# Kernel tuning notes

Hardware: AMD Instinct MI355X
Metric: run time of the kernel (lower is better)

The kernel has to match this reference:

```python
import jax, jax.numpy as jnp
import numpy as np

N = 262144   # total sentences
B = 16384    # number of bags
D = 768      # relation_dim
C = 53       # num_classes


def setup_inputs() -> dict:
    key = jax.random.key(0)
    k1, k2, k3, k4 = jax.random.split(key, 4)
    x = jax.random.normal(k1, (N, D), dtype=jnp.float32)
    # xavier_uniform-like init for the relation embedding matrix [C, D]
    limit = float(np.sqrt(6.0 / (C + D)))
    rel_weight = jax.random.uniform(k2, (C, D), dtype=jnp.float32, minval=-limit, maxval=limit)
    bias = jax.random.normal(k3, (C,), dtype=jnp.float32)
    query = jax.random.randint(k4, (N,), 0, C, dtype=jnp.int32)
    # uniform bag boundaries: 0, 16, 32, ..., N  (len B+1)
    input_scope = (jnp.arange(B + 1, dtype=jnp.int32) * (N // B)).astype(jnp.int32)
    return {"x": x, "rel_weight": rel_weight, "bias": bias,
            "input_scope": input_scope, "query": query}


def reference(x, rel_weight, bias, input_scope, query):
    n = x.shape[0]
    num_bags = input_scope.shape[0] - 1
    # segment id of each sentence from bag boundaries (ragged -> segment form)
    seg = jnp.searchsorted(input_scope[1:], jnp.arange(n, dtype=input_scope.dtype), side="right")
    # _train_logits: per-sentence attention score <x_i, rel_emb[query_i]>
    att = jnp.sum(x * rel_weight[query], axis=1)                  # [N]
    # segment-stable softmax within each bag
    m = jax.ops.segment_max(att, seg, num_segments=num_bags)      # [B]
    e = jnp.exp(att - m[seg])                                     # [N]
    z = jax.ops.segment_sum(e, seg, num_segments=num_bags)        # [B]
    w = e / z[seg]                                                # [N]
    # attention-weighted bag representation
    repre = jax.ops.segment_sum(x * w[:, None], seg, num_segments=num_bags)  # [B, D]
    # _logits: bag representation -> class logits
    logits = repre @ rel_weight.T + bias                          # [B, C]
    return logits
```

## Files before the change

### kernel.cpp

```cpp
#include <hip/hip_runtime.h>
#include <hip/hip_bf16.h>

#define DIM    768
#define NC     53
#define NCP    64
#define MTB    256
#define NTH    512
#define NSTEPS 24

typedef __attribute__((ext_vector_type(8))) short short8;
typedef __attribute__((ext_vector_type(4))) float f32x4;

static __device__ inline unsigned short f2bf(float f) {
    unsigned u = __float_as_uint(f);
    u += 0x7fff + ((u >> 16) & 1);
    return (unsigned short)(u >> 16);
}

__global__ void wconv_kernel(const float* __restrict__ W, unsigned short* __restrict__ Wt) {
    const int idx = blockIdx.x * 256 + threadIdx.x;
    if (idx >= NCP * DIM) return;
    const int c = idx / DIM, k = idx - c * DIM;
    Wt[idx] = f2bf((c < NC) ? W[c * DIM + k] : 0.f);
}

static __device__ inline short8 cvt8(const float4 a, const float4 b) {
    union { __hip_bfloat162 h[4]; short8 s; } u;
    u.h[0] = __float22bfloat162_rn(make_float2(a.x, a.y));
    u.h[1] = __float22bfloat162_rn(make_float2(a.z, a.w));
    u.h[2] = __float22bfloat162_rn(make_float2(b.x, b.y));
    u.h[3] = __float22bfloat162_rn(make_float2(b.z, b.w));
    return u.s;
}

__global__ __launch_bounds__(NTH, 4) void bag_attn_mfma2(
    const float* __restrict__ x,
    const unsigned short* __restrict__ Wt,
    const float* __restrict__ bias,
    const int*   __restrict__ query,
    float*       __restrict__ out)
{
    __shared__ float att_sm[16][16];

    const int t   = threadIdx.x;
    const int w   = t >> 6;
    const int l   = t & 63;
    const int blk = blockIdx.x;
    const int row_g = blk * MTB;

    const int r16 = l & 15;
    const int kq  = l >> 4;

    const float4* a0p = reinterpret_cast<const float4*>(x)
                      + (size_t)(row_g + 32 * w + r16) * (DIM / 4) + kq * 2;
    const float4* a1p = a0p + 16 * (DIM / 4);
    const unsigned short* wb = Wt + r16 * DIM + kq * 8;

    f32x4 acc[2][4];
    #pragma unroll
    for (int mi = 0; mi < 2; ++mi)
        #pragma unroll
        for (int ni = 0; ni < 4; ++ni)
            acc[mi][ni] = (f32x4){0.f, 0.f, 0.f, 0.f};

    float4 P0a = a0p[0], P0b = a0p[1], P1a = a1p[0], P1b = a1p[1];
    float4 Q0a = a0p[8], Q0b = a0p[9], Q1a = a1p[8], Q1b = a1p[9];

    #pragma unroll
    for (int kk = 0; kk < NSTEPS; kk += 2) {
        {
            const short8 af0 = cvt8(P0a, P0b);
            const short8 af1 = cvt8(P1a, P1b);
            if (kk + 2 < NSTEPS) {
                P0a = a0p[(kk + 2) * 8 + 0]; P0b = a0p[(kk + 2) * 8 + 1];
                P1a = a1p[(kk + 2) * 8 + 0]; P1b = a1p[(kk + 2) * 8 + 1];
            }
            #pragma unroll
            for (int ni = 0; ni < 4; ++ni) {
                const short8 bf = *reinterpret_cast<const short8*>(
                    wb + ni * 16 * DIM + kk * 32);
                acc[0][ni] = __builtin_amdgcn_mfma_f32_16x16x32_bf16(af0, bf, acc[0][ni], 0, 0, 0);
                acc[1][ni] = __builtin_amdgcn_mfma_f32_16x16x32_bf16(af1, bf, acc[1][ni], 0, 0, 0);
            }
        }
        {
            const short8 ag0 = cvt8(Q0a, Q0b);
            const short8 ag1 = cvt8(Q1a, Q1b);
            if (kk + 3 < NSTEPS) {
                Q0a = a0p[(kk + 3) * 8 + 0]; Q0b = a0p[(kk + 3) * 8 + 1];
                Q1a = a1p[(kk + 3) * 8 + 0]; Q1b = a1p[(kk + 3) * 8 + 1];
            }
            #pragma unroll
            for (int ni = 0; ni < 4; ++ni) {
                const short8 bf = *reinterpret_cast<const short8*>(
                    wb + ni * 16 * DIM + (kk + 1) * 32);
                acc[0][ni] = __builtin_amdgcn_mfma_f32_16x16x32_bf16(ag0, bf, acc[0][ni], 0, 0, 0);
                acc[1][ni] = __builtin_amdgcn_mfma_f32_16x16x32_bf16(ag1, bf, acc[1][ni], 0, 0, 0);
            }
        }
    }

    #pragma unroll
    for (int mi = 0; mi < 2; ++mi) {
        #pragma unroll
        for (int r = 0; r < 4; ++r) {
            const int s_loc = (kq << 2) + r;
            const int q = query[row_g + 32 * w + 16 * mi + s_loc];
            if ((q & 15) == r16) {
                float v = acc[mi][0][r];
                if ((q >> 4) == 1) v = acc[mi][1][r];
                if ((q >> 4) == 2) v = acc[mi][2][r];
                if ((q >> 4) == 3) v = acc[mi][3][r];
                att_sm[2 * w + mi][s_loc] = v;
            }
        }
    }

    #pragma unroll
    for (int mi = 0; mi < 2; ++mi) {
        const int bag = 2 * w + mi;
        const float4* a4 = reinterpret_cast<const float4*>(&att_sm[bag][0]);
        const float4 A0 = a4[0], A1 = a4[1], A2 = a4[2], A3 = a4[3];
        float mx = fmaxf(fmaxf(fmaxf(A0.x, A0.y), fmaxf(A0.z, A0.w)),
                  fmaxf(fmaxf(fmaxf(A1.x, A1.y), fmaxf(A1.z, A1.w)),
                  fmaxf(fmaxf(fmaxf(A2.x, A2.y), fmaxf(A2.z, A2.w)),
                        fmaxf(fmaxf(A3.x, A3.y), fmaxf(A3.z, A3.w)))));
        float zz = __expf(A0.x-mx)+__expf(A0.y-mx)+__expf(A0.z-mx)+__expf(A0.w-mx)
                 + __expf(A1.x-mx)+__expf(A1.y-mx)+__expf(A1.z-mx)+__expf(A1.w-mx)
                 + __expf(A2.x-mx)+__expf(A2.y-mx)+__expf(A2.z-mx)+__expf(A2.w-mx)
                 + __expf(A3.x-mx)+__expf(A3.y-mx)+__expf(A3.z-mx)+__expf(A3.w-mx);
        const float inv = 1.f / zz;
        float4 As = A0;
        if (kq == 1) As = A1;
        if (kq == 2) As = A2;
        if (kq == 3) As = A3;
        const float w0 = __expf(As.x - mx) * inv;
        const float w1 = __expf(As.y - mx) * inv;
        const float w2 = __expf(As.z - mx) * inv;
        const float w3 = __expf(As.w - mx) * inv;
        #pragma unroll
        for (int ni = 0; ni < 4; ++ni) {
            float p = w0 * acc[mi][ni][0] + w1 * acc[mi][ni][1]
                    + w2 * acc[mi][ni][2] + w3 * acc[mi][ni][3];
            p += __shfl_xor(p, 16, 64);
            p += __shfl_xor(p, 32, 64);
            if (l < 16) {
                const int c = 16 * ni + l;
                if (c < NC)
                    out[(size_t)(blk * 16 + bag) * NC + c] = p + bias[c];
            }
        }
    }
}

extern "C" void kernel_launch(void* const* d_in, const int* in_sizes, int n_in,
                              void* d_out, int out_size, void* d_ws, size_t ws_size,
                              hipStream_t stream) {
    const float* x     = (const float*)d_in[0];
    const float* W     = (const float*)d_in[1];
    const float* bias  = (const float*)d_in[2];
    const int*   query = (const int*)d_in[4];
    float* out = (float*)d_out;

    unsigned short* Wt = (unsigned short*)d_ws;

    const int nrows = in_sizes[0] / DIM;
    const int nblk  = nrows / MTB;

    wconv_kernel<<<(NCP * DIM + 255) / 256, 256, 0, stream>>>(W, Wt);
    bag_attn_mfma2<<<nblk, NTH, 0, stream>>>(x, Wt, bias, query, out);
}
```

Measured before the change: 212.6 us.

## Split block into producer and consumer waves with double-buffered LDS staging

The block is split into two roles. Four producer waves load x from global memory, convert it to bf16 and write it into a double-buffered, padded LDS tile, one bag per phase. Four consumer waves each compute one 16-class slice of the logits with MFMA, then run the bag softmax and write the weighted output. The aim is to overlap global loads with MFMA work, but it adds a block-wide barrier every phase and leaves half the waves doing no compute.

```diff
diff --git a/kernel.cpp b/kernel.cpp
--- a/kernel.cpp
+++ b/kernel.cpp
@@ -1,12 +1,14 @@
 #include <hip/hip_runtime.h>
 #include <hip/hip_bf16.h>
 
-#define DIM    768
-#define NC     53
-#define NCP    64
-#define MTB    256
-#define NTH    512
-#define NSTEPS 24
+#define DIM   768
+#define NC    53
+#define NCP   64
+#define MTB   256
+#define NTH   512
+#define NPH   16
+#define LSTR  776
+#define LBUF  (16 * LSTR)
 
 typedef __attribute__((ext_vector_type(8))) short short8;
 typedef __attribute__((ext_vector_type(4))) float f32x4;
@@ -24,130 +26,127 @@
     Wt[idx] = f2bf((c < NC) ? W[c * DIM + k] : 0.f);
 }
 
-static __device__ inline short8 cvt8(const float4 a, const float4 b) {
-    union { __hip_bfloat162 h[4]; short8 s; } u;
-    u.h[0] = __float22bfloat162_rn(make_float2(a.x, a.y));
-    u.h[1] = __float22bfloat162_rn(make_float2(a.z, a.w));
-    u.h[2] = __float22bfloat162_rn(make_float2(b.x, b.y));
-    u.h[3] = __float22bfloat162_rn(make_float2(b.z, b.w));
-    return u.s;
+static __device__ inline void cvt_store8(unsigned short* dst, const float4 v) {
+    union { __hip_bfloat162 h[2]; uint2 u; } z;
+    z.h[0] = __float22bfloat162_rn(make_float2(v.x, v.y));
+    z.h[1] = __float22bfloat162_rn(make_float2(v.z, v.w));
+    *reinterpret_cast<uint2*>(dst) = z.u;
 }
 
-__global__ __launch_bounds__(NTH, 4) void bag_attn_mfma2(
+__global__ __launch_bounds__(NTH) void bag_attn_pc(
     const float* __restrict__ x,
     const unsigned short* __restrict__ Wt,
     const float* __restrict__ bias,
     const int*   __restrict__ query,
     float*       __restrict__ out)
 {
-    __shared__ float att_sm[16][16];
+    __shared__ __align__(16) unsigned short Ab[2][LBUF];
+    __shared__ float att_sm[2][16];
+    __shared__ int   qbuf[MTB];
 
     const int t   = threadIdx.x;
     const int w   = t >> 6;
     const int l   = t & 63;
+    const int r16 = l & 15;
+    const int kq  = l >> 4;
     const int blk = blockIdx.x;
     const int row_g = blk * MTB;
 
-    const int r16 = l & 15;
-    const int kq  = l >> 4;
+    if (t < MTB) qbuf[t] = query[row_g + t];
 
-    const float4* a0p = reinterpret_cast<const float4*>(x)
-                      + (size_t)(row_g + 32 * w + r16) * (DIM / 4) + kq * 2;
-    const float4* a1p = a0p + 16 * (DIM / 4);
-    const unsigned short* wb = Wt + r16 * DIM + kq * 8;
+    const bool prod = (w >= 4);
+    const int  pid  = w - 4;
 
-    f32x4 acc[2][4];
-    #pragma unroll
-    for (int mi = 0; mi < 2; ++mi)
+    const float* xb = x + (size_t)row_g * DIM;
+    float4 rg[12];
+    int    lofs[12];
+    if (prod) {
         #pragma unroll
-        for (int ni = 0; ni < 4; ++ni)
-            acc[mi][ni] = (f32x4){0.f, 0.f, 0.f, 0.f};
+        for (int j = 0; j < 12; ++j) {
+            const int c = pid * 12 + j;
+            lofs[j] = (c / 3) * LSTR + (c % 3) * 256 + l * 4;
+        }
+        #pragma unroll
+        for (int j = 0; j < 12; ++j) {
+            const int c = pid * 12 + j;
+            rg[j] = *reinterpret_cast<const float4*>(
+                xb + (size_t)(c / 3) * DIM + (c % 3) * 256 + l * 4);
+        }
+        #pragma unroll
+        for (int j = 0; j < 12; ++j)
+            cvt_store8(&Ab[0][lofs[j]], rg[j]);
+        #pragma unroll
+        for (int j = 0; j < 12; ++j) {
+            const int c = pid * 12 + j;
+            rg[j] = *reinterpret_cast<const float4*>(
+                xb + (size_t)(16 + c / 3) * DIM + (c % 3) * 256 + l * 4);
+        }
+    }
+    const unsigned short* wb = Wt + (size_t)(16 * w + r16) * DIM + kq * 8;
 
-    float4 P0a = a0p[0], P0b = a0p[1], P1a = a1p[0], P1b = a1p[1];
-    float4 Q0a = a0p[8], Q0b = a0p[9], Q1a = a1p[8], Q1b = a1p[9];
+    __syncthreads();
 
-    #pragma unroll
-    for (int kk = 0; kk < NSTEPS; kk += 2) {
-        {
-            const short8 af0 = cvt8(P0a, P0b);
-            const short8 af1 = cvt8(P1a, P1b);
-            if (kk + 2 < NSTEPS) {
-                P0a = a0p[(kk + 2) * 8 + 0]; P0b = a0p[(kk + 2) * 8 + 1];
-                P1a = a1p[(kk + 2) * 8 + 0]; P1b = a1p[(kk + 2) * 8 + 1];
+    for (int p = 0; p < NPH; ++p) {
+        f32x4 acc = (f32x4){0.f, 0.f, 0.f, 0.f};
+        if (prod) {
+            if (p + 1 < NPH) {
+                #pragma unroll
+                for (int j = 0; j < 12; ++j)
+                    cvt_store8(&Ab[(p + 1) & 1][lofs[j]], rg[j]);
+            }
+            if (p + 2 < NPH) {
+                #pragma unroll
+                for (int j = 0; j < 12; ++j) {
+                    const int c = pid * 12 + j;
+                    rg[j] = *reinterpret_cast<const float4*>(
+                        xb + (size_t)((p + 2) * 16 + c / 3) * DIM
+                           + (c % 3) * 256 + l * 4);
+                }
+            }
+        } else {
+            const unsigned short* ab = &Ab[p & 1][r16 * LSTR + kq * 8];
+            #pragma unroll
+            for (int kk = 0; kk < 24; ++kk) {
+                const short8 a = *reinterpret_cast<const short8*>(ab + kk * 32);
+                const short8 b = *reinterpret_cast<const short8*>(wb + kk * 32);
+                acc = __builtin_amdgcn_mfma_f32_16x16x32_bf16(a, b, acc, 0, 0, 0);
             }
             #pragma unroll
-            for (int ni = 0; ni < 4; ++ni) {
-                const short8 bf = *reinterpret_cast<const short8*>(
-                    wb + ni * 16 * DIM + kk * 32);
-                acc[0][ni] = __builtin_amdgcn_mfma_f32_16x16x32_bf16(af0, bf, acc[0][ni], 0, 0, 0);
-                acc[1][ni] = __builtin_amdgcn_mfma_f32_16x16x32_bf16(af1, bf, acc[1][ni], 0, 0, 0);
+            for (int r = 0; r < 4; ++r) {
+                const int s = kq * 4 + r;
+                const int q = qbuf[p * 16 + s];
+                if ((q >> 4) == w && (q & 15) == r16)
+                    att_sm[p & 1][s] = acc[r];
             }
         }
-        {
-            const short8 ag0 = cvt8(Q0a, Q0b);
-            const short8 ag1 = cvt8(Q1a, Q1b);
-            if (kk + 3 < NSTEPS) {
-                Q0a = a0p[(kk + 3) * 8 + 0]; Q0b = a0p[(kk + 3) * 8 + 1];
-                Q1a = a1p[(kk + 3) * 8 + 0]; Q1b = a1p[(kk + 3) * 8 + 1];
-            }
-            #pragma unroll
-            for (int ni = 0; ni < 4; ++ni) {
-                const short8 bf = *reinterpret_cast<const short8*>(
-                    wb + ni * 16 * DIM + (kk + 1) * 32);
-                acc[0][ni] = __builtin_amdgcn_mfma_f32_16x16x32_bf16(ag0, bf, acc[0][ni], 0, 0, 0);
-                acc[1][ni] = __builtin_amdgcn_mfma_f32_16x16x32_bf16(ag1, bf, acc[1][ni], 0, 0, 0);
-            }
-        }
-    }
-
-    #pragma unroll
-    for (int mi = 0; mi < 2; ++mi) {
-        #pragma unroll
-        for (int r = 0; r < 4; ++r) {
-            const int s_loc = (kq << 2) + r;
-            const int q = query[row_g + 32 * w + 16 * mi + s_loc];
-            if ((q & 15) == r16) {
-                float v = acc[mi][0][r];
-                if ((q >> 4) == 1) v = acc[mi][1][r];
-                if ((q >> 4) == 2) v = acc[mi][2][r];
-                if ((q >> 4) == 3) v = acc[mi][3][r];
-                att_sm[2 * w + mi][s_loc] = v;
-            }
-        }
-    }
-
-    #pragma unroll
-    for (int mi = 0; mi < 2; ++mi) {
-        const int bag = 2 * w + mi;
-        const float4* a4 = reinterpret_cast<const float4*>(&att_sm[bag][0]);
-        const float4 A0 = a4[0], A1 = a4[1], A2 = a4[2], A3 = a4[3];
-        float mx = fmaxf(fmaxf(fmaxf(A0.x, A0.y), fmaxf(A0.z, A0.w)),
-                  fmaxf(fmaxf(fmaxf(A1.x, A1.y), fmaxf(A1.z, A1.w)),
-                  fmaxf(fmaxf(fmaxf(A2.x, A2.y), fmaxf(A2.z, A2.w)),
-                        fmaxf(fmaxf(A3.x, A3.y), fmaxf(A3.z, A3.w)))));
-        float zz = __expf(A0.x-mx)+__expf(A0.y-mx)+__expf(A0.z-mx)+__expf(A0.w-mx)
-                 + __expf(A1.x-mx)+__expf(A1.y-mx)+__expf(A1.z-mx)+__expf(A1.w-mx)
-                 + __expf(A2.x-mx)+__expf(A2.y-mx)+__expf(A2.z-mx)+__expf(A2.w-mx)
-                 + __expf(A3.x-mx)+__expf(A3.y-mx)+__expf(A3.z-mx)+__expf(A3.w-mx);
-        const float inv = 1.f / zz;
-        float4 As = A0;
-        if (kq == 1) As = A1;
-        if (kq == 2) As = A2;
-        if (kq == 3) As = A3;
-        const float w0 = __expf(As.x - mx) * inv;
-        const float w1 = __expf(As.y - mx) * inv;
-        const float w2 = __expf(As.z - mx) * inv;
-        const float w3 = __expf(As.w - mx) * inv;
-        #pragma unroll
-        for (int ni = 0; ni < 4; ++ni) {
-            float p = w0 * acc[mi][ni][0] + w1 * acc[mi][ni][1]
-                    + w2 * acc[mi][ni][2] + w3 * acc[mi][ni][3];
-            p += __shfl_xor(p, 16, 64);
-            p += __shfl_xor(p, 32, 64);
+        __syncthreads();
+        if (!prod) {
+            const float4* a4 = reinterpret_cast<const float4*>(&att_sm[p & 1][0]);
+            const float4 A0 = a4[0], A1 = a4[1], A2 = a4[2], A3 = a4[3];
+            float mx = fmaxf(fmaxf(fmaxf(A0.x, A0.y), fmaxf(A0.z, A0.w)),
+                      fmaxf(fmaxf(fmaxf(A1.x, A1.y), fmaxf(A1.z, A1.w)),
+                      fmaxf(fmaxf(fmaxf(A2.x, A2.y), fmaxf(A2.z, A2.w)),
+                            fmaxf(fmaxf(A3.x, A3.y), fmaxf(A3.z, A3.w)))));
+            float zz = __expf(A0.x-mx)+__expf(A0.y-mx)+__expf(A0.z-mx)+__expf(A0.w-mx)
+                     + __expf(A1.x-mx)+__expf(A1.y-mx)+__expf(A1.z-mx)+__expf(A1.w-mx)
+                     + __expf(A2.x-mx)+__expf(A2.y-mx)+__expf(A2.z-mx)+__expf(A2.w-mx)
+                     + __expf(A3.x-mx)+__expf(A3.y-mx)+__expf(A3.z-mx)+__expf(A3.w-mx);
+            const float inv = 1.f / zz;
+            float4 As = A0;
+            if (kq == 1) As = A1;
+            if (kq == 2) As = A2;
+            if (kq == 3) As = A3;
+            const float e0 = __expf(As.x - mx) * inv;
+            const float e1 = __expf(As.y - mx) * inv;
+            const float e2 = __expf(As.z - mx) * inv;
+            const float e3 = __expf(As.w - mx) * inv;
+            float pv = e0 * acc[0] + e1 * acc[1] + e2 * acc[2] + e3 * acc[3];
+            pv += __shfl_xor(pv, 16, 64);
+            pv += __shfl_xor(pv, 32, 64);
             if (l < 16) {
-                const int c = 16 * ni + l;
+                const int c = 16 * w + l;
                 if (c < NC)
-                    out[(size_t)(blk * 16 + bag) * NC + c] = p + bias[c];
+                    out[(size_t)(blk * 16 + p) * NC + c] = pv + bias[c];
             }
         }
     }
@@ -168,5 +167,5 @@
     const int nblk  = nrows / MTB;
 
     wconv_kernel<<<(NCP * DIM + 255) / 256, 256, 0, stream>>>(W, Wt);
-    bag_attn_mfma2<<<nblk, NTH, 0, stream>>>(x, Wt, bias, query, out);
+    bag_attn_pc<<<nblk, NTH, 0, stream>>>(x, Wt, bias, query, out);
 }
```

Result: slower. 318.8 us (+50.0%).

## Stage x tiles through per-wave double-buffered LDS with coalesced row loads

Applied to the files above, without the earlier changes.

Each wave now loads its 32 rows of x with 8 lanes covering 128 contiguous bytes per row. It converts them to bf16 and writes them into a padded, double-buffered LDS tile, then reads MFMA A fragments back from LDS. The old scheme had each lane fetch scattered 32-byte pieces straight into fragments. Because each wave reads only the rows it wrote, no block barriers are needed. Weight fragment loads are also software-pipelined, one step ahead. The cost is extra LDS traffic and about 40KB of LDS per block, which may limit occupancy.

```diff
diff --git a/kernel.cpp b/kernel.cpp
--- a/kernel.cpp
+++ b/kernel.cpp
@@ -6,7 +6,10 @@
 #define NCP    64
 #define MTB    256
 #define NTH    512
+#define KSTEP  32
 #define NSTEPS 24
+#define APAD   40
+#define D4     (DIM/4)
 
 typedef __attribute__((ext_vector_type(8))) short short8;
 typedef __attribute__((ext_vector_type(4))) float f32x4;
@@ -24,37 +27,34 @@
     Wt[idx] = f2bf((c < NC) ? W[c * DIM + k] : 0.f);
 }
 
-static __device__ inline short8 cvt8(const float4 a, const float4 b) {
-    union { __hip_bfloat162 h[4]; short8 s; } u;
-    u.h[0] = __float22bfloat162_rn(make_float2(a.x, a.y));
-    u.h[1] = __float22bfloat162_rn(make_float2(a.z, a.w));
-    u.h[2] = __float22bfloat162_rn(make_float2(b.x, b.y));
-    u.h[3] = __float22bfloat162_rn(make_float2(b.z, b.w));
-    return u.s;
+static __device__ inline void cvt_store8(unsigned short* dst, const float4 v) {
+    union { __hip_bfloat162 h[2]; uint2 u; } z;
+    z.h[0] = __float22bfloat162_rn(make_float2(v.x, v.y));
+    z.h[1] = __float22bfloat162_rn(make_float2(v.z, v.w));
+    *reinterpret_cast<uint2*>(dst) = z.u;
 }
 
-__global__ __launch_bounds__(NTH, 4) void bag_attn_mfma2(
+__global__ __launch_bounds__(NTH, 4) void bag_attn_nobar(
     const float* __restrict__ x,
     const unsigned short* __restrict__ Wt,
     const float* __restrict__ bias,
     const int*   __restrict__ query,
     float*       __restrict__ out)
 {
+    __shared__ __align__(16) unsigned short Ab[2][MTB * APAD];
     __shared__ float att_sm[16][16];
 
     const int t   = threadIdx.x;
     const int w   = t >> 6;
     const int l   = t & 63;
+    const int r16 = l & 15;
+    const int kq  = l >> 4;
     const int blk = blockIdx.x;
     const int row_g = blk * MTB;
 
-    const int r16 = l & 15;
-    const int kq  = l >> 4;
-
-    const float4* a0p = reinterpret_cast<const float4*>(x)
-                      + (size_t)(row_g + 32 * w + r16) * (DIM / 4) + kq * 2;
-    const float4* a1p = a0p + 16 * (DIM / 4);
-    const unsigned short* wb = Wt + r16 * DIM + kq * 8;
+    const float4* xp = reinterpret_cast<const float4*>(x)
+                     + (size_t)(row_g + 32 * w + (l >> 3)) * D4 + (l & 7);
+    const int lofs = (32 * w + (l >> 3)) * APAD + (l & 7) * 4;
 
     f32x4 acc[2][4];
     #pragma unroll
@@ -63,42 +63,61 @@
         for (int ni = 0; ni < 4; ++ni)
             acc[mi][ni] = (f32x4){0.f, 0.f, 0.f, 0.f};
 
-    float4 P0a = a0p[0], P0b = a0p[1], P1a = a1p[0], P1b = a1p[1];
-    float4 Q0a = a0p[8], Q0b = a0p[9], Q1a = a1p[8], Q1b = a1p[9];
+    const unsigned short* wbase = Wt + (size_t)r16 * DIM + kq * 8;
 
-    #pragma unroll
+#define LOADB(B, kk)                                                     \
+    _Pragma("unroll")                                                    \
+    for (int ni = 0; ni < 4; ++ni)                                       \
+        B[ni] = *reinterpret_cast<const short8*>(                        \
+            wbase + (size_t)(16 * ni) * DIM + (kk) * KSTEP);
+
+#define LOADX(R, kk)                                                     \
+    _Pragma("unroll")                                                    \
+    for (int i = 0; i < 4; ++i)                                          \
+        R[i] = xp[(size_t)i * 8 * D4 + (kk) * 8];
+
+#define STOREX(R, buf)                                                   \
+    _Pragma("unroll")                                                    \
+    for (int i = 0; i < 4; ++i)                                          \
+        cvt_store8(&Ab[buf][lofs + i * 8 * APAD], R[i]);
+
+#define COMPUTE(p, B)                                                    \
+    {                                                                    \
+        short8 afr[2];                                                   \
+        _Pragma("unroll")                                                \
+        for (int mi = 0; mi < 2; ++mi)                                   \
+            afr[mi] = *reinterpret_cast<const short8*>(                  \
+                &Ab[p][(32 * w + 16 * mi + r16) * APAD + kq * 8]);       \
+        _Pragma("unroll")                                                \
+        for (int mi = 0; mi < 2; ++mi)                                   \
+            _Pragma("unroll")                                            \
+            for (int ni = 0; ni < 4; ++ni)                               \
+                acc[mi][ni] = __builtin_amdgcn_mfma_f32_16x16x32_bf16(   \
+                    afr[mi], B[ni], acc[mi][ni], 0, 0, 0);               \
+    }
+
+    short8 bP[4], bQ[4];
+    float4 rA[4], rB[4];
+
+    LOADB(bP, 0);
+    LOADX(rA, 0);
+    LOADX(rB, 1);
+    STOREX(rA, 0);
+
     for (int kk = 0; kk < NSTEPS; kk += 2) {
-        {
-            const short8 af0 = cvt8(P0a, P0b);
-            const short8 af1 = cvt8(P1a, P1b);
-            if (kk + 2 < NSTEPS) {
-                P0a = a0p[(kk + 2) * 8 + 0]; P0b = a0p[(kk + 2) * 8 + 1];
-                P1a = a1p[(kk + 2) * 8 + 0]; P1b = a1p[(kk + 2) * 8 + 1];
-            }
-            #pragma unroll
-            for (int ni = 0; ni < 4; ++ni) {
-                const short8 bf = *reinterpret_cast<const short8*>(
-                    wb + ni * 16 * DIM + kk * 32);
-                acc[0][ni] = __builtin_amdgcn_mfma_f32_16x16x32_bf16(af0, bf, acc[0][ni], 0, 0, 0);
-                acc[1][ni] = __builtin_amdgcn_mfma_f32_16x16x32_bf16(af1, bf, acc[1][ni], 0, 0, 0);
-            }
-        }
-        {
-            const short8 ag0 = cvt8(Q0a, Q0b);
-            const short8 ag1 = cvt8(Q1a, Q1b);
-            if (kk + 3 < NSTEPS) {
-                Q0a = a0p[(kk + 3) * 8 + 0]; Q0b = a0p[(kk + 3) * 8 + 1];
-                Q1a = a1p[(kk + 3) * 8 + 0]; Q1b = a1p[(kk + 3) * 8 + 1];
-            }
-            #pragma unroll
-            for (int ni = 0; ni < 4; ++ni) {
-                const short8 bf = *reinterpret_cast<const short8*>(
-                    wb + ni * 16 * DIM + (kk + 1) * 32);
-                acc[0][ni] = __builtin_amdgcn_mfma_f32_16x16x32_bf16(ag0, bf, acc[0][ni], 0, 0, 0);
-                acc[1][ni] = __builtin_amdgcn_mfma_f32_16x16x32_bf16(ag1, bf, acc[1][ni], 0, 0, 0);
-            }
-        }
+        LOADB(bQ, kk + 1);
+        if (kk + 2 < NSTEPS) LOADX(rA, kk + 2);
+        COMPUTE(0, bP);
+        STOREX(rB, 1);
+        if (kk + 2 < NSTEPS) LOADB(bP, kk + 2);
+        if (kk + 3 < NSTEPS) LOADX(rB, kk + 3);
+        COMPUTE(1, bQ);
+        if (kk + 2 < NSTEPS) STOREX(rA, 0);
     }
+#undef LOADB
+#undef LOADX
+#undef STOREX
+#undef COMPUTE
 
     #pragma unroll
     for (int mi = 0; mi < 2; ++mi) {
@@ -134,14 +153,14 @@
         if (kq == 1) As = A1;
         if (kq == 2) As = A2;
         if (kq == 3) As = A3;
-        const float w0 = __expf(As.x - mx) * inv;
-        const float w1 = __expf(As.y - mx) * inv;
-        const float w2 = __expf(As.z - mx) * inv;
-        const float w3 = __expf(As.w - mx) * inv;
+        const float e0 = __expf(As.x - mx) * inv;
+        const float e1 = __expf(As.y - mx) * inv;
+        const float e2 = __expf(As.z - mx) * inv;
+        const float e3 = __expf(As.w - mx) * inv;
         #pragma unroll
         for (int ni = 0; ni < 4; ++ni) {
-            float p = w0 * acc[mi][ni][0] + w1 * acc[mi][ni][1]
-                    + w2 * acc[mi][ni][2] + w3 * acc[mi][ni][3];
+            float p = e0 * acc[mi][ni][0] + e1 * acc[mi][ni][1]
+                    + e2 * acc[mi][ni][2] + e3 * acc[mi][ni][3];
             p += __shfl_xor(p, 16, 64);
             p += __shfl_xor(p, 32, 64);
             if (l < 16) {
@@ -168,5 +187,5 @@
     const int nblk  = nrows / MTB;
 
     wconv_kernel<<<(NCP * DIM + 255) / 256, 256, 0, stream>>>(W, Wt);
-    bag_attn_mfma2<<<nblk, NTH, 0, stream>>>(x, Wt, bias, query, out);
+    bag_attn_nobar<<<nblk, NTH, 0, stream>>>(x, Wt, bias, query, out);
 }
```

New measurement: 200.9 us. -5.5%, faster.

## Stage x tiles into LDS via async global_load_lds with double buffering

Applied to the files above, without the earlier changes.

Instead of loading x directly into registers with software prefetch, each block now streams 32-column x tiles into a double-buffered LDS area using global_load_lds DMA with an XOR swizzle, then reads bf16-converted fragments from LDS for MFMA. Blocks shrink to 64 rows and 128 threads (4 bags), and the query values are cached in shared memory. The aim is better latency hiding and memory throughput on the bandwidth-bound x stream, at the cost of two barriers per K step and more, smaller blocks.

```diff
diff --git a/kernel.cpp b/kernel.cpp
--- a/kernel.cpp
+++ b/kernel.cpp
@@ -4,9 +4,11 @@
 #define DIM    768
 #define NC     53
 #define NCP    64
-#define MTB    256
-#define NTH    512
+#define MTB    64
+#define NTH    128
+#define KSTEP  32
 #define NSTEPS 24
+#define D4v    192
 
 typedef __attribute__((ext_vector_type(8))) short short8;
 typedef __attribute__((ext_vector_type(4))) float f32x4;
@@ -33,28 +35,29 @@
     return u.s;
 }
 
-__global__ __launch_bounds__(NTH, 4) void bag_attn_mfma2(
+__global__ __launch_bounds__(NTH) void bag_attn_dma(
     const float* __restrict__ x,
     const unsigned short* __restrict__ Wt,
     const float* __restrict__ bias,
     const int*   __restrict__ query,
     float*       __restrict__ out)
 {
-    __shared__ float att_sm[16][16];
+    __shared__ __align__(16) float AbF[2][MTB * 32];
+    __shared__ float att_sm[4][16];
+    __shared__ int   qbuf[MTB];
 
     const int t   = threadIdx.x;
     const int w   = t >> 6;
     const int l   = t & 63;
+    const int r16 = l & 15;
+    const int kq  = l >> 4;
     const int blk = blockIdx.x;
     const int row_g = blk * MTB;
 
-    const int r16 = l & 15;
-    const int kq  = l >> 4;
+    if (t < MTB) qbuf[t] = query[row_g + t];
 
-    const float4* a0p = reinterpret_cast<const float4*>(x)
-                      + (size_t)(row_g + 32 * w + r16) * (DIM / 4) + kq * 2;
-    const float4* a1p = a0p + 16 * (DIM / 4);
-    const unsigned short* wb = Wt + r16 * DIM + kq * 8;
+    const float* xg = x + (size_t)(row_g + 32 * w + (l >> 3)) * DIM
+                    + (((l & 7) ^ (l >> 3)) << 2);
 
     f32x4 acc[2][4];
     #pragma unroll
@@ -63,49 +66,60 @@
         for (int ni = 0; ni < 4; ++ni)
             acc[mi][ni] = (f32x4){0.f, 0.f, 0.f, 0.f};
 
-    float4 P0a = a0p[0], P0b = a0p[1], P1a = a1p[0], P1b = a1p[1];
-    float4 Q0a = a0p[8], Q0b = a0p[9], Q1a = a1p[8], Q1b = a1p[9];
+#define STAGE(buf, kk)                                                        \
+    _Pragma("unroll")                                                         \
+    for (int i = 0; i < 4; ++i)                                               \
+        __builtin_amdgcn_global_load_lds(                                     \
+            (const __attribute__((address_space(1))) void*)                   \
+                (xg + (size_t)i * 8 * DIM + (kk) * KSTEP),                    \
+            (__attribute__((address_space(3))) void*)                         \
+                (&AbF[buf][(32 * w + 8 * i) * 32]),                           \
+            16, 0, 0);
 
-    #pragma unroll
+#define COMPUTE(p, kk)                                                        \
+    {                                                                         \
+        short8 bfr[4];                                                        \
+        _Pragma("unroll")                                                     \
+        for (int ni = 0; ni < 4; ++ni)                                        \
+            bfr[ni] = *reinterpret_cast<const short8*>(                       \
+                Wt + ((16 * ni + r16) * DIM + (kk) * KSTEP + kq * 8));        \
+        short8 afr[2];                                                        \
+        _Pragma("unroll")                                                     \
+        for (int mi = 0; mi < 2; ++mi) {                                      \
+            const float4* rowp = reinterpret_cast<const float4*>(             \
+                &AbF[p][(32 * w + 16 * mi + r16) * 32]);                      \
+            const float4 v0 = rowp[(2 * kq + 0) ^ (r16 & 7)];                 \
+            const float4 v1 = rowp[(2 * kq + 1) ^ (r16 & 7)];                 \
+            afr[mi] = cvt8(v0, v1);                                           \
+        }                                                                     \
+        _Pragma("unroll")                                                     \
+        for (int mi = 0; mi < 2; ++mi)                                        \
+            _Pragma("unroll")                                                 \
+            for (int ni = 0; ni < 4; ++ni)                                    \
+                acc[mi][ni] = __builtin_amdgcn_mfma_f32_16x16x32_bf16(        \
+                    afr[mi], bfr[ni], acc[mi][ni], 0, 0, 0);                  \
+    }
+
+    STAGE(0, 0);
+    __syncthreads();
+
     for (int kk = 0; kk < NSTEPS; kk += 2) {
-        {
-            const short8 af0 = cvt8(P0a, P0b);
-            const short8 af1 = cvt8(P1a, P1b);
-            if (kk + 2 < NSTEPS) {
-                P0a = a0p[(kk + 2) * 8 + 0]; P0b = a0p[(kk + 2) * 8 + 1];
-                P1a = a1p[(kk + 2) * 8 + 0]; P1b = a1p[(kk + 2) * 8 + 1];
-            }
-            #pragma unroll
-            for (int ni = 0; ni < 4; ++ni) {
-                const short8 bf = *reinterpret_cast<const short8*>(
-                    wb + ni * 16 * DIM + kk * 32);
-                acc[0][ni] = __builtin_amdgcn_mfma_f32_16x16x32_bf16(af0, bf, acc[0][ni], 0, 0, 0);
-                acc[1][ni] = __builtin_amdgcn_mfma_f32_16x16x32_bf16(af1, bf, acc[1][ni], 0, 0, 0);
-            }
-        }
-        {
-            const short8 ag0 = cvt8(Q0a, Q0b);
-            const short8 ag1 = cvt8(Q1a, Q1b);
-            if (kk + 3 < NSTEPS) {
-                Q0a = a0p[(kk + 3) * 8 + 0]; Q0b = a0p[(kk + 3) * 8 + 1];
-                Q1a = a1p[(kk + 3) * 8 + 0]; Q1b = a1p[(kk + 3) * 8 + 1];
-            }
-            #pragma unroll
-            for (int ni = 0; ni < 4; ++ni) {
-                const short8 bf = *reinterpret_cast<const short8*>(
-                    wb + ni * 16 * DIM + (kk + 1) * 32);
-                acc[0][ni] = __builtin_amdgcn_mfma_f32_16x16x32_bf16(ag0, bf, acc[0][ni], 0, 0, 0);
-                acc[1][ni] = __builtin_amdgcn_mfma_f32_16x16x32_bf16(ag1, bf, acc[1][ni], 0, 0, 0);
-            }
-        }
+        if (kk + 1 < NSTEPS) STAGE(1, kk + 1);
+        COMPUTE(0, kk);
+        __syncthreads();
+        if (kk + 2 < NSTEPS) STAGE(0, kk + 2);
+        COMPUTE(1, kk + 1);
+        __syncthreads();
     }
+#undef STAGE
+#undef COMPUTE
 
     #pragma unroll
     for (int mi = 0; mi < 2; ++mi) {
         #pragma unroll
         for (int r = 0; r < 4; ++r) {
             const int s_loc = (kq << 2) + r;
-            const int q = query[row_g + 32 * w + 16 * mi + s_loc];
+            const int q = qbuf[32 * w + 16 * mi + s_loc];
             if ((q & 15) == r16) {
                 float v = acc[mi][0][r];
                 if ((q >> 4) == 1) v = acc[mi][1][r];
@@ -134,20 +148,20 @@
         if (kq == 1) As = A1;
         if (kq == 2) As = A2;
         if (kq == 3) As = A3;
-        const float w0 = __expf(As.x - mx) * inv;
-        const float w1 = __expf(As.y - mx) * inv;
-        const float w2 = __expf(As.z - mx) * inv;
-        const float w3 = __expf(As.w - mx) * inv;
+        const float e0 = __expf(As.x - mx) * inv;
+        const float e1 = __expf(As.y - mx) * inv;
+        const float e2 = __expf(As.z - mx) * inv;
+        const float e3 = __expf(As.w - mx) * inv;
         #pragma unroll
         for (int ni = 0; ni < 4; ++ni) {
-            float p = w0 * acc[mi][ni][0] + w1 * acc[mi][ni][1]
-                    + w2 * acc[mi][ni][2] + w3 * acc[mi][ni][3];
+            float p = e0 * acc[mi][ni][0] + e1 * acc[mi][ni][1]
+                    + e2 * acc[mi][ni][2] + e3 * acc[mi][ni][3];
             p += __shfl_xor(p, 16, 64);
             p += __shfl_xor(p, 32, 64);
             if (l < 16) {
                 const int c = 16 * ni + l;
                 if (c < NC)
-                    out[(size_t)(blk * 16 + bag) * NC + c] = p + bias[c];
+                    out[(size_t)(blk * 4 + bag) * NC + c] = p + bias[c];
             }
         }
     }
@@ -168,5 +182,5 @@
     const int nblk  = nrows / MTB;
 
     wconv_kernel<<<(NCP * DIM + 255) / 256, 256, 0, stream>>>(W, Wt);
-    bag_attn_mfma2<<<nblk, NTH, 0, stream>>>(x, Wt, bias, query, out);
+    bag_attn_dma<<<nblk, NTH, 0, stream>>>(x, Wt, bias, query, out);
 }
```

Measured after the change: 204.5 us. 1.04x faster.
